# Kernel optimization log

Hardware: AMD Instinct MI355X
Metric: run time of the kernel (lower is better)

Reference implementation:

```python
import jax, jax.numpy as jnp
import numpy as np

D_MODEL = 1024
D_INNER = 2048      # expand=2 * d_model
HEADDIM = 64
NHEADS = D_INNER // HEADDIM   # 32 (ssm heads)
D_STATE = 128
D_CONV = 4
CHUNK = 256
D_IN_PROJ = 2 * D_INNER + 2 * D_STATE + NHEADS
CONV_DIM = D_INNER + 2 * D_STATE


def setup_inputs() -> dict:
    key = jax.random.key(0)
    ks = jax.random.split(key, 8)
    sc = lambda f: 1.0 / np.sqrt(f)
    dt_init = jax.random.uniform(ks[3], (NHEADS,), minval=0.001, maxval=0.1)
    return {
        "x": jax.random.normal(ks[0], (2, 4096, D_MODEL), jnp.float32),
        "W_in": jax.random.normal(ks[1], (D_MODEL, D_IN_PROJ), jnp.float32) * sc(D_MODEL),
        "conv_w": jax.random.normal(ks[2], (CONV_DIM, D_CONV), jnp.float32) * sc(D_CONV),
        "conv_b": jnp.zeros((CONV_DIM,), jnp.float32),
        "dt_bias": jnp.log(jnp.expm1(dt_init)),            # inverse softplus
        "A_log": jnp.log(jax.random.uniform(ks[4], (NHEADS,), minval=1.0, maxval=16.0)),
        "D": jnp.ones((NHEADS,), jnp.float32),
        "norm_w": jnp.ones((D_INNER,), jnp.float32),
        "W_out": jax.random.normal(ks[5], (D_INNER, D_MODEL), jnp.float32) * sc(D_INNER),
    }


def _segsum(a):
    # a: (..., T) -> (..., T, T) lower-triangular segment sums, -inf above diag
    T = a.shape[-1]
    cs = jnp.cumsum(a, axis=-1)
    diff = cs[..., :, None] - cs[..., None, :]
    mask = jnp.tril(jnp.ones((T, T), bool))
    return jnp.where(mask, diff, -jnp.inf)


def _ssd(x, A, B, C):
    # x: (b,L,h,p) already scaled by dt; A: (b,L,h) = dt*A_head; B,C: (b,L,n)
    b, L, h, p = x.shape
    nc = L // CHUNK
    xc = x.reshape(b, nc, CHUNK, h, p)
    Ac = A.reshape(b, nc, CHUNK, h).transpose(0, 3, 1, 2)      # (b,h,nc,cl)
    Bc = B.reshape(b, nc, CHUNK, -1)
    Cc = C.reshape(b, nc, CHUNK, -1)
    Acs = jnp.cumsum(Ac, axis=-1)
    # intra-chunk (diagonal) term
    Ldec = jnp.exp(_segsum(Ac))                                # (b,h,nc,cl,cl)
    Yd = jnp.einsum('bcln,bcsn,bhcls,bcshp->bclhp', Cc, Bc, Ldec, xc)
    # chunk end states
    decay_states = jnp.exp(Acs[..., -1:] - Acs)                # (b,h,nc,cl)
    states = jnp.einsum('bcln,bhcl,bclhp->bchpn', Bc, decay_states, xc)
    # inter-chunk recurrence (zero initial state)
    states = jnp.concatenate([jnp.zeros_like(states[:, :1]), states], axis=1)
    A_chunk = jnp.pad(Acs[..., -1], ((0, 0), (0, 0), (1, 0)))  # (b,h,nc+1)
    decay_chunk = jnp.exp(_segsum(A_chunk))                    # (b,h,nc+1,nc+1)
    states = jnp.einsum('bhzc,bchpn->bzhpn', decay_chunk, states)[:, :-1]
    # state -> output term
    out_decay = jnp.exp(Acs)                                   # (b,h,nc,cl)
    Yo = jnp.einsum('bcln,bchpn,bhcl->bclhp', Cc, states, out_decay)
    return (Yd + Yo).reshape(b, L, h, p)


def reference(x, W_in, conv_w, conv_b, dt_bias, A_log, D, norm_w, W_out):
    b, L, _ = x.shape
    zxbcdt = x @ W_in                                          # (b,L,4384)
    z, xBC, dt = jnp.split(zxbcdt, [D_INNER, 2 * D_INNER + 2 * D_STATE], axis=-1)
    # causal depthwise conv1d + silu
    xp = jnp.pad(xBC, ((0, 0), (D_CONV - 1, 0), (0, 0)))
    conv = sum(xp[:, k:k + L] * conv_w[:, k] for k in range(D_CONV)) + conv_b
    xBC = jax.nn.silu(conv)
    xs, B, C = jnp.split(xBC, [D_INNER, D_INNER + D_STATE], axis=-1)
    dt = jax.nn.softplus(dt + dt_bias)                         # (b,L,h)
    A = -jnp.exp(A_log)                                        # (h,)
    xh = xs.reshape(b, L, NHEADS, HEADDIM)
    y = _ssd(xh * dt[..., None], dt * A, B, C)                 # (b,L,h,p)
    y = y + xh * D[None, None, :, None]                        # D skip per head
    y = y.reshape(b, L, D_INNER)
    # gated RMSNorm
    u = y * jax.nn.silu(z)
    u = u * jax.lax.rsqrt(jnp.mean(u * u, axis=-1, keepdims=True) + 1e-5) * norm_w
    return u @ W_out
```

## Files before the change

kernel.cpp:

```cpp
#include <hip/hip_runtime.h>
#include <math.h>

#define B_ 2
#define L_ 4096
#define DM 1024
#define DI 2048
#define HD 64
#define NH 32
#define DS 128
#define CH 256
#define NC 16
#define DPROJ 4384
#define CONVD 2304
#define NGEMM 4352

typedef unsigned short u16;
typedef unsigned int u32;
typedef __attribute__((ext_vector_type(8))) short bf16x8;
typedef __attribute__((ext_vector_type(4))) float f32x4;

__device__ __forceinline__ float silu_(float x) { return x / (1.0f + __expf(-x)); }
__device__ __forceinline__ float us2f(u16 u) {
  union { u32 i; float f; } c; c.i = ((u32)u) << 16; return c.f;
}
__device__ __forceinline__ u16 f2us(float f) {
  union { float f; u32 i; } c; c.f = f;
  u32 i = c.i;
  return (u16)((i + 0x7FFFu + ((i >> 16) & 1u)) >> 16);
}
__device__ __forceinline__ void unpack8(uint4 v, float* o) {
  o[0] = us2f(v.x & 0xffffu); o[1] = us2f(v.x >> 16);
  o[2] = us2f(v.y & 0xffffu); o[3] = us2f(v.y >> 16);
  o[4] = us2f(v.z & 0xffffu); o[5] = us2f(v.z >> 16);
  o[6] = us2f(v.w & 0xffffu); o[7] = us2f(v.w >> 16);
}
__device__ __forceinline__ bf16x8 scale8(bf16x8 a, float s) {
  bf16x8 r;
#pragma unroll
  for (int j = 0; j < 8; ++j) r[j] = (short)f2us(us2f((u16)a[j]) * s);
  return r;
}
__device__ __forceinline__ void gload16(const u16* g, u16* l) {
  __builtin_amdgcn_global_load_lds(
      (const __attribute__((address_space(1))) void*)g,
      (__attribute__((address_space(3))) void*)l, 16, 0, 0);
}

__global__ __launch_bounds__(256) void cvt_t_k(const float* __restrict__ W,
                                               u16* __restrict__ Wt,
                                               int ldW, int ldT) {
  __shared__ float tile[64][65];
  const int t = threadIdx.x;
  const int n0 = blockIdx.x * 64, k0 = blockIdx.y * 64;
#pragma unroll
  for (int i = 0; i < 16; ++i) {
    int j = i * 256 + t;
    int kk = j >> 6, nn = j & 63;
    tile[kk][nn] = W[(size_t)(k0 + kk) * ldW + n0 + nn];
  }
  __syncthreads();
#pragma unroll
  for (int i = 0; i < 16; ++i) {
    int j = i * 256 + t;
    int nn = j >> 6, kk = j & 63;
    Wt[(size_t)(n0 + nn) * ldT + k0 + kk] = f2us(tile[kk][nn]);
  }
}

template <int KDIM, int NTN, int EPI>
__global__ __launch_bounds__(256) void gemm_bf16_k(const u16* __restrict__ A,
                                                   const u16* __restrict__ Bt,
                                                   u16* __restrict__ zb,
                                                   u16* __restrict__ xraw,
                                                   float* __restrict__ outf,
                                                   int nwg) {
  __shared__ u16 pool[(EPI == 1) ? 17408 : 16384];
  u16* Al = pool;
  u16* Bl = pool + 8192;
  const int t = threadIdx.x;
  const int wv = t >> 6, lane = t & 63;
  const int fr = lane & 15, oct = lane >> 4;
  const int wr = wv >> 1, wc = wv & 1;
  const int q = nwg >> 3;
  const int wg = (blockIdx.x & 7) * q + (blockIdx.x >> 3);
  const int bm = wg / NTN, bn = wg % NTN;
  const int m0 = bm * 128, n0 = bn * 128;

  const int lr = lane >> 3, ls = lane & 7;
  const int gslot = (ls ^ lr) * 8;

  f32x4 acc[4][4];
#pragma unroll
  for (int mm = 0; mm < 4; ++mm)
#pragma unroll
    for (int nn = 0; nn < 4; ++nn) acc[mm][nn] = (f32x4){0.f, 0.f, 0.f, 0.f};

  for (int k0 = 0; k0 < KDIM; k0 += 64) {
    if (k0) __syncthreads();
#pragma unroll
    for (int i = 0; i < 4; ++i) {
      const int rowA = wv * 32 + i * 8;
      gload16(&A[(size_t)(m0 + rowA + lr) * KDIM + k0 + gslot], &Al[rowA * 64]);
      gload16(&Bt[(size_t)(n0 + rowA + lr) * KDIM + k0 + gslot], &Bl[rowA * 64]);
    }
    __syncthreads();
#pragma unroll
    for (int kk = 0; kk < 2; ++kk) {
      bf16x8 af[4], bfr[4];
#pragma unroll
      for (int mm = 0; mm < 4; ++mm)
        af[mm] = *(const bf16x8*)&Al[(wr * 64 + mm * 16 + fr) * 64 +
                                     (((kk * 4 + oct) ^ (fr & 7)) * 8)];
#pragma unroll
      for (int nn = 0; nn < 4; ++nn)
        bfr[nn] = *(const bf16x8*)&Bl[(wc * 64 + nn * 16 + fr) * 64 +
                                      (((kk * 4 + oct) ^ (fr & 7)) * 8)];
#pragma unroll
      for (int mm = 0; mm < 4; ++mm)
#pragma unroll
        for (int nn = 0; nn < 4; ++nn)
          acc[mm][nn] = __builtin_amdgcn_mfma_f32_16x16x32_bf16(af[mm], bfr[nn],
                                                                acc[mm][nn], 0, 0, 0);
    }
  }

  if (EPI == 0) {
    const bool isz = (n0 < DI);
#pragma unroll
    for (int P = 0; P < 2; ++P) {
      __syncthreads();
      u16* Oh = pool;
      if (wr == P) {
#pragma unroll
        for (int mm = 0; mm < 4; ++mm)
#pragma unroll
          for (int i = 0; i < 4; ++i) {
            int rloc = mm * 16 + oct * 4 + i;
#pragma unroll
            for (int nn = 0; nn < 4; ++nn)
              Oh[rloc * 136 + wc * 64 + nn * 16 + fr] = f2us(acc[mm][nn][i]);
          }
      }
      __syncthreads();
#pragma unroll
      for (int p = 0; p < 4; ++p) {
        int e = p * 256 + t;
        int row = e >> 4, cs = (e & 15) * 8;
        uint4 v = *(const uint4*)&Oh[row * 136 + cs];
        size_t grow = m0 + P * 64 + row;
        int col = n0 + cs;
        if (isz) *(uint4*)&zb[grow * DI + col] = v;
        else     *(uint4*)&xraw[grow * CONVD + (col - DI)] = v;
      }
    }
  } else {
#pragma unroll
    for (int P = 0; P < 2; ++P) {
      __syncthreads();
      float* Of = (float*)pool;
      if (wr == P) {
#pragma unroll
        for (int mm = 0; mm < 4; ++mm)
#pragma unroll
          for (int i = 0; i < 4; ++i) {
            int rloc = mm * 16 + oct * 4 + i;
#pragma unroll
            for (int nn = 0; nn < 4; ++nn)
              Of[rloc * 132 + wc * 64 + nn * 16 + fr] = acc[mm][nn][i];
          }
      }
      __syncthreads();
#pragma unroll
      for (int p = 0; p < 8; ++p) {
        int e = p * 256 + t;
        int row = e >> 5, c4 = (e & 31) * 4;
        float4 v = *(const float4*)&Of[row * 132 + c4];
        *(float4*)&outf[(size_t)(m0 + P * 64 + row) * DM + n0 + c4] = v;
      }
    }
  }
}

__global__ __launch_bounds__(256) void dt_gemm_k(const float* __restrict__ x,
                                                 const float* __restrict__ W,
                                                 const float* __restrict__ dtb,
                                                 float* __restrict__ dtp,
                                                 u16* __restrict__ xb16) {
  __shared__ float xs[8 * 1024];
  const int t = threadIdx.x;
  const int row0 = blockIdx.x * 8;
#pragma unroll
  for (int i = 0; i < 8; ++i) {
    int j4 = i * 256 + t;
    float4 v = *(const float4*)&x[(size_t)row0 * DM + j4 * 4];
    *(float4*)&xs[j4 * 4] = v;
    u32 lo = (u32)f2us(v.x) | ((u32)f2us(v.y) << 16);
    u32 hi = (u32)f2us(v.z) | ((u32)f2us(v.w) << 16);
    *(uint2*)&xb16[(size_t)row0 * DM + j4 * 4] = make_uint2(lo, hi);
  }
  __syncthreads();
  const int r = t >> 5, h = t & 31;
  float a0 = 0.f, a1 = 0.f, a2 = 0.f, a3 = 0.f;
  const float* wcol = W + (DI + CONVD) + h;
  const float* xr = &xs[r * 1024];
  for (int k = 0; k < 1024; k += 4) {
    float4 xv = *(const float4*)&xr[k];
    a0 += xv.x * wcol[(size_t)(k + 0) * DPROJ];
    a1 += xv.y * wcol[(size_t)(k + 1) * DPROJ];
    a2 += xv.z * wcol[(size_t)(k + 2) * DPROJ];
    a3 += xv.w * wcol[(size_t)(k + 3) * DPROJ];
  }
  float v = (a0 + a1) + (a2 + a3) + dtb[h];
  dtp[(size_t)(row0 + r) * NH + h] = (v > 20.0f) ? v : log1pf(__expf(v));
}

__global__ __launch_bounds__(256) void conv_silu_k(const u16* __restrict__ xraw,
                                                   const float* __restrict__ cw,
                                                   const float* __restrict__ cb,
                                                   u16* __restrict__ xbc) {
  int idx = blockIdx.x * 256 + threadIdx.x;
  int ch8 = idx % (CONVD / 8);
  int bl = idx / (CONVD / 8);
  int l = bl & (L_ - 1);
  int ch = ch8 * 8;
  const u16* src = xraw + (size_t)bl * CONVD + ch;
  float a[8], o[8];
#pragma unroll
  for (int qq = 0; qq < 8; ++qq) a[qq] = cb[ch + qq];
  float w0[8], w1[8], w2[8], w3[8];
#pragma unroll
  for (int qq = 0; qq < 8; ++qq) {
    float4 w = *(const float4*)&cw[(ch + qq) * 4];
    w0[qq] = w.x; w1[qq] = w.y; w2[qq] = w.z; w3[qq] = w.w;
  }
  if (l >= 3) {
    uint4 v = *(const uint4*)&src[-3 * CONVD]; unpack8(v, o);
#pragma unroll
    for (int qq = 0; qq < 8; ++qq) a[qq] += o[qq] * w0[qq];
  }
  if (l >= 2) {
    uint4 v = *(const uint4*)&src[-2 * CONVD]; unpack8(v, o);
#pragma unroll
    for (int qq = 0; qq < 8; ++qq) a[qq] += o[qq] * w1[qq];
  }
  if (l >= 1) {
    uint4 v = *(const uint4*)&src[-CONVD]; unpack8(v, o);
#pragma unroll
    for (int qq = 0; qq < 8; ++qq) a[qq] += o[qq] * w2[qq];
  }
  {
    uint4 v = *(const uint4*)&src[0]; unpack8(v, o);
#pragma unroll
    for (int qq = 0; qq < 8; ++qq) a[qq] += o[qq] * w3[qq];
  }
  uint4 ov;
  ov.x = (u32)f2us(silu_(a[0])) | ((u32)f2us(silu_(a[1])) << 16);
  ov.y = (u32)f2us(silu_(a[2])) | ((u32)f2us(silu_(a[3])) << 16);
  ov.z = (u32)f2us(silu_(a[4])) | ((u32)f2us(silu_(a[5])) << 16);
  ov.w = (u32)f2us(silu_(a[6])) | ((u32)f2us(silu_(a[7])) << 16);
  *(uint4*)&xbc[(size_t)bl * CONVD + ch] = ov;
}

__global__ __launch_bounds__(256) void acs_k(const float* __restrict__ dtp,
                                             const float* __restrict__ A_log,
                                             float* __restrict__ Acs) {
  const int t = threadIdx.x;
  const int lane = t & 63, wv = t >> 6;
  const int idx = blockIdx.x * 4 + wv;
  const int h = (idx >> 4) & (NH - 1);
  const int c = idx & (NC - 1);
  const int b = idx >> 9;
  const float Ah = -__expf(A_log[h]);
  const size_t base = ((size_t)b * L_ + c * CH + lane * 4) * NH + h;
  float v0 = dtp[base] * Ah;
  float v1 = dtp[base + NH] * Ah;
  float v2 = dtp[base + 2 * NH] * Ah;
  float v3 = dtp[base + 3 * NH] * Ah;
  float c1 = v0 + v1, c2 = c1 + v2, c3 = c2 + v3;
  float tot = c3;
#pragma unroll
  for (int off = 1; off < 64; off <<= 1) {
    float p = __shfl_up(tot, off, 64);
    if (lane >= off) tot += p;
  }
  float excl = tot - c3;
  float4 ov = make_float4(excl + v0, excl + c1, excl + c2, excl + c3);
  *(float4*)&Acs[(size_t)idx * CH + lane * 4] = ov;
}

#define SLP 72
__global__ __launch_bounds__(256) void states_k(const u16* __restrict__ xbc,
                                                const float* __restrict__ dtp,
                                                const float* __restrict__ Acs,
                                                u16* __restrict__ st16) {
  __shared__ u16 BtT[128 * SLP];
  __shared__ u16 XtT[64 * SLP];
  const int t = threadIdx.x;
  const int wv = t >> 6, lane = t & 63;
  const int fr = lane & 15, oct = lane >> 4;
  const int h = blockIdx.x & 31, c = (blockIdx.x >> 5) & 15, b = blockIdx.x >> 9;
  const size_t acsb = (((size_t)b * NH + h) * NC + c) * CH;
  const float acs_last = Acs[acsb + (CH - 1)];
  const size_t rowbase = (size_t)b * L_ + c * CH;

  f32x4 acc[2][4];
#pragma unroll
  for (int mt = 0; mt < 2; ++mt)
#pragma unroll
    for (int pt = 0; pt < 4; ++pt) acc[mt][pt] = (f32x4){0.f, 0.f, 0.f, 0.f};

  for (int lt = 0; lt < 4; ++lt) {
    __syncthreads();
#pragma unroll
    for (int i = 0; i < 4; ++i) {
      int ci = i * 256 + t;
      int l = ci >> 4, nk = ci & 15;
      uint4 v = *(const uint4*)&xbc[(rowbase + lt * 64 + l) * CONVD + DI + nk * 8];
      u16 p8[8];
      p8[0] = (u16)(v.x & 0xffffu); p8[1] = (u16)(v.x >> 16);
      p8[2] = (u16)(v.y & 0xffffu); p8[3] = (u16)(v.y >> 16);
      p8[4] = (u16)(v.z & 0xffffu); p8[5] = (u16)(v.z >> 16);
      p8[6] = (u16)(v.w & 0xffffu); p8[7] = (u16)(v.w >> 16);
#pragma unroll
      for (int qq = 0; qq < 8; ++qq) {
        int r = nk * 8 + qq;
        BtT[r * SLP + ((((l >> 3) ^ (r >> 3)) & 7) << 3) + (l & 7)] = p8[qq];
      }
    }
#pragma unroll
    for (int i = 0; i < 2; ++i) {
      int ci = i * 256 + t;
      int l = ci >> 3, pk = ci & 7;
      size_t row = rowbase + lt * 64 + l;
      uint4 v = *(const uint4*)&xbc[row * CONVD + h * HD + pk * 8];
      float d = dtp[row * NH + h] * __expf(acs_last - Acs[acsb + lt * 64 + l]);
      float o[8]; unpack8(v, o);
#pragma unroll
      for (int qq = 0; qq < 8; ++qq) {
        int r = pk * 8 + qq;
        XtT[r * SLP + ((((l >> 3) ^ (r >> 3)) & 7) << 3) + (l & 7)] = f2us(o[qq] * d);
      }
    }
    __syncthreads();
    __builtin_amdgcn_s_setprio(1);
#pragma unroll
    for (int ks = 0; ks < 2; ++ks) {
      bf16x8 afr[2], bfr[4];
#pragma unroll
      for (int mt = 0; mt < 2; ++mt) {
        int r = wv * 32 + mt * 16 + fr;
        afr[mt] = *(const bf16x8*)&BtT[r * SLP + ((((ks * 4 + oct) ^ (r >> 3)) & 7) << 3)];
      }
#pragma unroll
      for (int pt = 0; pt < 4; ++pt) {
        int r = pt * 16 + fr;
        bfr[pt] = *(const bf16x8*)&XtT[r * SLP + ((((ks * 4 + oct) ^ (r >> 3)) & 7) << 3)];
      }
#pragma unroll
      for (int mt = 0; mt < 2; ++mt)
#pragma unroll
        for (int pt = 0; pt < 4; ++pt)
          acc[mt][pt] = __builtin_amdgcn_mfma_f32_16x16x32_bf16(afr[mt], bfr[pt],
                                                                acc[mt][pt], 0, 0, 0);
    }
    __builtin_amdgcn_s_setprio(0);
  }
  size_t sbase = (((size_t)b * NC + c) * NH + h) * (size_t)(HD * DS);
#pragma unroll
  for (int mt = 0; mt < 2; ++mt)
#pragma unroll
    for (int pt = 0; pt < 4; ++pt) {
      int p = pt * 16 + fr;
      int n0 = wv * 32 + mt * 16 + oct * 4;
      u32 lo = (u32)f2us(acc[mt][pt][0]) | ((u32)f2us(acc[mt][pt][1]) << 16);
      u32 hi = (u32)f2us(acc[mt][pt][2]) | ((u32)f2us(acc[mt][pt][3]) << 16);
      *(uint2*)&st16[sbase + (size_t)p * DS + n0] = make_uint2(lo, hi);
    }
}

__global__ __launch_bounds__(256) void scan_k(u16* __restrict__ st16,
                                              const float* __restrict__ Acs) {
  const int t = threadIdx.x;
  const int seg = blockIdx.x & 15;
  const int bh = blockIdx.x >> 4;
  const int h = bh & 31, b = bh >> 5;
  const int e2 = seg * 256 + t;
  const size_t acssb = ((size_t)b * NH + h) * NC * CH;
  float run0 = 0.0f, run1 = 0.0f;
#pragma unroll
  for (int c = 0; c < NC; ++c) {
    float dAl = __expf(Acs[acssb + (size_t)c * CH + (CH - 1)]);
    size_t e = (((size_t)b * NC + c) * NH + h) * (size_t)(HD * DS) + e2 * 2;
    u32 v = *(const u32*)&st16[e];
    float s0 = us2f((u16)(v & 0xffffu)), s1 = us2f((u16)(v >> 16));
    *(u32*)&st16[e] = (u32)f2us(run0) | ((u32)f2us(run1) << 16);
    run0 = fmaf(dAl, run0, s0);
    run1 = fmaf(dAl, run1, s1);
  }
}

#define SP 72
#define XOFF 8192
#define POFF 12800
__global__ __launch_bounds__(512, 4) void ssd_out_k(const u16* __restrict__ xbc,
                                                    const float* __restrict__ dtp,
                                                    const float* __restrict__ Acs,
                                                    const u16* __restrict__ st16,
                                                    const float* __restrict__ Dvec,
                                                    u16* __restrict__ y) {
  __shared__ u16 pool[31232];
  __shared__ float acs_s[256];
  const int t = threadIdx.x;
  const int w = t >> 6, lane = t & 63;
  const int fr = lane & 15, oct = lane >> 4;
  const int h = blockIdx.x & 31, c = (blockIdx.x >> 5) & 15, b = blockIdx.x >> 9;
  const size_t acsb = (((size_t)b * NH + h) * NC + c) * CH;
  const size_t rowbase = (size_t)b * L_ + c * CH;
  if (t < 256) acs_s[t] = Acs[acsb + t];
  const size_t sb = (((size_t)b * NC + c) * NH + h) * (size_t)(HD * DS);
#pragma unroll
  for (int i = 0; i < 2; ++i) {
    int ci = i * 512 + t; int p = ci >> 4, nk = ci & 15;
    uint4 v = *(const uint4*)&st16[sb + (size_t)p * DS + nk * 8];
    *(uint4*)&pool[p * 136 + nk * 8] = v;
  }
  __syncthreads();
  bf16x8 ca[2][4];
#pragma unroll
  for (int mt = 0; mt < 2; ++mt)
#pragma unroll
    for (int kk = 0; kk < 4; ++kk)
      ca[mt][kk] = *(const bf16x8*)&xbc[(rowbase + w * 32 + mt * 16 + fr) * CONVD +
                                        DI + DS + kk * 32 + oct * 8];
  f32x4 acc_y[2][4];
#pragma unroll
  for (int mt = 0; mt < 2; ++mt)
#pragma unroll
    for (int pp4 = 0; pp4 < 4; ++pp4) acc_y[mt][pp4] = (f32x4){0.f, 0.f, 0.f, 0.f};

  {
    float eL0 = __expf(acs_s[w * 32 + fr]);
    float eL1 = __expf(acs_s[w * 32 + 16 + fr]);
    __builtin_amdgcn_s_setprio(1);
#pragma unroll
    for (int kk = 0; kk < 4; ++kk) {
      bf16x8 c0 = scale8(ca[0][kk], eL0);
      bf16x8 c1 = scale8(ca[1][kk], eL1);
#pragma unroll
      for (int pp4 = 0; pp4 < 4; ++pp4) {
        bf16x8 sf = *(const bf16x8*)&pool[(pp4 * 16 + fr) * 136 + kk * 32 + oct * 8];
        acc_y[0][pp4] = __builtin_amdgcn_mfma_f32_16x16x32_bf16(c0, sf, acc_y[0][pp4], 0, 0, 0);
        acc_y[1][pp4] = __builtin_amdgcn_mfma_f32_16x16x32_bf16(c1, sf, acc_y[1][pp4], 0, 0, 0);
      }
    }
    __builtin_amdgcn_s_setprio(0);
  }

  const int stmax = w >> 1, delta = (w & 1) << 5;
  for (int st = 0; st < 4; ++st) {
    __syncthreads();
#pragma unroll
    for (int i = 0; i < 2; ++i) {
      int ci = i * 512 + t; int ll = ci >> 4, ck = ci & 15;
      uint4 v = *(const uint4*)&xbc[(rowbase + st * 64 + ll) * CONVD + DI + ck * 8];
      *(uint4*)&pool[ll * 128 + ((ck * 8) ^ ((ll & 7) << 3))] = v;
    }
    {
      int s = t >> 3, pk = t & 7;
      size_t row = rowbase + st * 64 + s;
      uint4 v = *(const uint4*)&xbc[row * CONVD + h * HD + pk * 8];
      float d = dtp[row * NH + h];
      float o[8]; unpack8(v, o);
#pragma unroll
      for (int qq = 0; qq < 8; ++qq) {
        int r = pk * 8 + qq;
        pool[XOFF + r * SP + ((((s >> 3) ^ (r >> 3)) & 7) << 3) + (s & 7)] = f2us(o[qq] * d);
      }
    }
    __syncthreads();
    if (st > stmax) continue;
    const bool diag = (st == stmax);
#pragma unroll
    for (int ss4 = 0; ss4 < 4; ++ss4) {
      bf16x8 bbf[4];
#pragma unroll
      for (int kk = 0; kk < 4; ++kk)
        bbf[kk] = *(const bf16x8*)&pool[(ss4 * 16 + fr) * 128 +
                                        ((kk * 32 + oct * 8) ^ ((fr & 7) << 3))];
      int s_in = ss4 * 16 + fr;
      float aS = acs_s[st * 64 + s_in];
#pragma unroll
      for (int mt = 0; mt < 2; ++mt) {
        f32x4 sacc = (f32x4){0.f, 0.f, 0.f, 0.f};
        __builtin_amdgcn_s_setprio(1);
#pragma unroll
        for (int kk = 0; kk < 4; ++kk)
          sacc = __builtin_amdgcn_mfma_f32_16x16x32_bf16(ca[mt][kk], bbf[kk], sacc, 0, 0, 0);
        __builtin_amdgcn_s_setprio(0);
#pragma unroll
        for (int i = 0; i < 4; ++i) {
          int r = mt * 16 + oct * 4 + i;
          float aL = acs_s[w * 32 + r];
          float wgt = (!diag || (s_in <= r + delta)) ? __expf(aL - aS) : 0.0f;
          pool[POFF + w * 2304 + r * SP + s_in] = f2us(sacc[i] * wgt);
        }
      }
    }
    bf16x8 pa[2][2];
#pragma unroll
    for (int mt = 0; mt < 2; ++mt)
#pragma unroll
      for (int k2 = 0; k2 < 2; ++k2)
        pa[mt][k2] = *(const bf16x8*)&pool[POFF + w * 2304 + (mt * 16 + fr) * SP +
                                           k2 * 32 + oct * 8];
    __builtin_amdgcn_s_setprio(1);
#pragma unroll
    for (int pp4 = 0; pp4 < 4; ++pp4) {
      int rx = pp4 * 16 + fr, xg = rx >> 3;
      bf16x8 xb0 = *(const bf16x8*)&pool[XOFF + rx * SP + (((oct) ^ xg) & 7) * 8];
      bf16x8 xb1 = *(const bf16x8*)&pool[XOFF + rx * SP + (((4 + oct) ^ xg) & 7) * 8];
#pragma unroll
      for (int mt = 0; mt < 2; ++mt) {
        acc_y[mt][pp4] = __builtin_amdgcn_mfma_f32_16x16x32_bf16(pa[mt][0], xb0, acc_y[mt][pp4], 0, 0, 0);
        acc_y[mt][pp4] = __builtin_amdgcn_mfma_f32_16x16x32_bf16(pa[mt][1], xb1, acc_y[mt][pp4], 0, 0, 0);
      }
    }
    __builtin_amdgcn_s_setprio(0);
  }

  const float Dh = Dvec[h];
#pragma unroll
  for (int mt = 0; mt < 2; ++mt)
#pragma unroll
    for (int i = 0; i < 4; ++i) {
      size_t row = rowbase + w * 32 + mt * 16 + oct * 4 + i;
#pragma unroll
      for (int pp4 = 0; pp4 < 4; ++pp4) {
        int col = h * HD + pp4 * 16 + fr;
        float xs = us2f(xbc[row * CONVD + col]);
        y[row * DI + col] = f2us(acc_y[mt][pp4][i] + Dh * xs);
      }
    }
}

__global__ __launch_bounds__(256) void gnorm_k(const u16* __restrict__ zb,
                                               const float* __restrict__ nw,
                                               u16* __restrict__ y) {
  const int row = blockIdx.x, t = threadIdx.x;
  const u16* zr = zb + (size_t)row * DI;
  u16* yr = y + (size_t)row * DI;
  uint4 zv = *(const uint4*)&zr[t * 8];
  uint4 yv = *(const uint4*)&yr[t * 8];
  float uz[8], uy[8];
  unpack8(zv, uz); unpack8(yv, uy);
  float u[8], ssum = 0.0f;
#pragma unroll
  for (int j = 0; j < 8; ++j) { u[j] = uy[j] * silu_(uz[j]); ssum += u[j] * u[j]; }
#pragma unroll
  for (int off = 32; off >= 1; off >>= 1) ssum += __shfl_xor(ssum, off, 64);
  __shared__ float red[4];
  if ((t & 63) == 0) red[t >> 6] = ssum;
  __syncthreads();
  float sc = rsqrtf((red[0] + red[1] + red[2] + red[3]) * (1.0f / DI) + 1e-5f);
  float4 w0 = *(const float4*)&nw[t * 8];
  float4 w1 = *(const float4*)&nw[t * 8 + 4];
  float o0 = u[0] * sc * w0.x, o1 = u[1] * sc * w0.y, o2 = u[2] * sc * w0.z, o3 = u[3] * sc * w0.w;
  float o4 = u[4] * sc * w1.x, o5 = u[5] * sc * w1.y, o6 = u[6] * sc * w1.z, o7 = u[7] * sc * w1.w;
  uint4 ov;
  ov.x = (u32)f2us(o0) | ((u32)f2us(o1) << 16);
  ov.y = (u32)f2us(o2) | ((u32)f2us(o3) << 16);
  ov.z = (u32)f2us(o4) | ((u32)f2us(o5) << 16);
  ov.w = (u32)f2us(o6) | ((u32)f2us(o7) << 16);
  *(uint4*)&yr[t * 8] = ov;
}

extern "C" void kernel_launch(void* const* d_in, const int* in_sizes, int n_in,
                              void* d_out, int out_size, void* d_ws, size_t ws_size,
                              hipStream_t stream) {
  const float* x      = (const float*)d_in[0];
  const float* W_in   = (const float*)d_in[1];
  const float* conv_w = (const float*)d_in[2];
  const float* conv_b = (const float*)d_in[3];
  const float* dt_b   = (const float*)d_in[4];
  const float* A_log  = (const float*)d_in[5];
  const float* Dvec   = (const float*)d_in[6];
  const float* norm_w = (const float*)d_in[7];
  const float* W_out  = (const float*)d_in[8];
  float* out = (float*)d_out;

  u16* zb       = (u16*)d_ws;
  u16* xbc      = zb + (size_t)B_ * L_ * DI;
  float* dtp    = (float*)(xbc + (size_t)B_ * L_ * CONVD);
  float* Acs    = dtp + (size_t)B_ * L_ * NH;
  u16* stregion = (u16*)(Acs + (size_t)B_ * NH * L_);
  u16* uni      = stregion + (size_t)B_ * NC * NH * HD * DS * 2;
  u16* xraw = uni;
  u16* y    = uni;

  u16* xb16     = stregion;
  u16* wint     = stregion + (size_t)B_ * L_ * DM;
  u16* states16 = stregion;
  u16* woutt    = stregion;

  const int Mrows = B_ * L_;

  dt_gemm_k<<<Mrows / 8, 256, 0, stream>>>(x, W_in, dt_b, dtp, xb16);
  cvt_t_k<<<dim3(NGEMM / 64, DM / 64), 256, 0, stream>>>(W_in, wint, DPROJ, DM);

  const int nwg_in = (Mrows / 128) * (NGEMM / 128);
  gemm_bf16_k<DM, NGEMM / 128, 0><<<nwg_in, 256, 0, stream>>>(
      xb16, wint, zb, xraw, nullptr, nwg_in);

  conv_silu_k<<<(Mrows * (CONVD / 8)) / 256, 256, 0, stream>>>(xraw, conv_w, conv_b, xbc);
  acs_k<<<(B_ * NH * NC) / 4, 256, 0, stream>>>(dtp, A_log, Acs);
  states_k<<<B_ * NC * NH, 256, 0, stream>>>(xbc, dtp, Acs, states16);
  scan_k<<<B_ * NH * 16, 256, 0, stream>>>(states16, Acs);
  ssd_out_k<<<B_ * NC * NH, 512, 0, stream>>>(xbc, dtp, Acs, states16, Dvec, y);
  gnorm_k<<<Mrows, 256, 0, stream>>>(zb, norm_w, y);

  cvt_t_k<<<dim3(DM / 64, DI / 64), 256, 0, stream>>>(W_out, woutt, DM, DI);
  const int nwg_out = (Mrows / 128) * (DM / 128);
  gemm_bf16_k<DI, DM / 128, 1><<<nwg_out, 256, 0, stream>>>(
      y, woutt, nullptr, nullptr, out, nwg_out);
}
```

Before: 348.1 us.

## Use 256x128 tiles for input GEMM and pair-row packed LDS transposes

Adds a dedicated in-projection GEMM kernel with 512-thread blocks computing 256x128 output tiles, so each B tile is reused across twice as many rows, and raises MFMA wave priority during the math. In states_k and ssd_out_k, each thread now handles two consecutive rows and writes packed 32-bit pairs into the transposed LDS tiles, halving the number of scattered 16-bit LDS stores. Both kernels also remap block indices with an XCD-style swizzle. The larger GEMM tile uses more LDS and registers per block, which may lower occupancy.

```diff
diff --git a/kernel.cpp b/kernel.cpp
--- a/kernel.cpp
+++ b/kernel.cpp
@@ -34,6 +34,12 @@
   o[4] = us2f(v.z & 0xffffu); o[5] = us2f(v.z >> 16);
   o[6] = us2f(v.w & 0xffffu); o[7] = us2f(v.w >> 16);
 }
+__device__ __forceinline__ void unpk16(uint4 v, u16* o) {
+  o[0] = (u16)(v.x & 0xffffu); o[1] = (u16)(v.x >> 16);
+  o[2] = (u16)(v.y & 0xffffu); o[3] = (u16)(v.y >> 16);
+  o[4] = (u16)(v.z & 0xffffu); o[5] = (u16)(v.z >> 16);
+  o[6] = (u16)(v.w & 0xffffu); o[7] = (u16)(v.w >> 16);
+}
 __device__ __forceinline__ bf16x8 scale8(bf16x8 a, float s) {
   bf16x8 r;
 #pragma unroll
@@ -67,14 +73,102 @@
   }
 }
 
-template <int KDIM, int NTN, int EPI>
+__global__ __launch_bounds__(512, 4) void gemm_in_k(const u16* __restrict__ A,
+                                                    const u16* __restrict__ Bt,
+                                                    u16* __restrict__ zb,
+                                                    u16* __restrict__ xraw,
+                                                    int nwg) {
+  __shared__ u16 pool[24576];
+  u16* Al = pool;
+  u16* Bl = pool + 16384;
+  const int t = threadIdx.x;
+  const int w = t >> 6, lane = t & 63;
+  const int fr = lane & 15, oct = lane >> 4;
+  const int wm = w >> 1, wn = w & 1;
+  const int q = nwg >> 3;
+  const int wg = (blockIdx.x & 7) * q + (blockIdx.x >> 3);
+  const int bm = wg / (NGEMM / 128), bn = wg % (NGEMM / 128);
+  const int m0 = bm * 256, n0 = bn * 128;
+  const int lr = lane >> 3, ls = lane & 7;
+  const int gslot = (ls ^ lr) * 8;
+
+  f32x4 acc[4][4];
+#pragma unroll
+  for (int mm = 0; mm < 4; ++mm)
+#pragma unroll
+    for (int nn = 0; nn < 4; ++nn) acc[mm][nn] = (f32x4){0.f, 0.f, 0.f, 0.f};
+
+  for (int k0 = 0; k0 < DM; k0 += 64) {
+    if (k0) __syncthreads();
+#pragma unroll
+    for (int i = 0; i < 4; ++i) {
+      const int rowA = w * 32 + i * 8;
+      gload16(&A[(size_t)(m0 + rowA + lr) * DM + k0 + gslot], &Al[rowA * 64]);
+    }
+#pragma unroll
+    for (int i = 0; i < 2; ++i) {
+      const int rowB = w * 16 + i * 8;
+      gload16(&Bt[(size_t)(n0 + rowB + lr) * DM + k0 + gslot], &Bl[rowB * 64]);
+    }
+    __syncthreads();
+#pragma unroll
+    for (int kk = 0; kk < 2; ++kk) {
+      bf16x8 af[4], bfr[4];
+#pragma unroll
+      for (int mm = 0; mm < 4; ++mm)
+        af[mm] = *(const bf16x8*)&Al[(wm * 64 + mm * 16 + fr) * 64 +
+                                     (((kk * 4 + oct) ^ (fr & 7)) * 8)];
+#pragma unroll
+      for (int nn = 0; nn < 4; ++nn)
+        bfr[nn] = *(const bf16x8*)&Bl[(wn * 64 + nn * 16 + fr) * 64 +
+                                      (((kk * 4 + oct) ^ (fr & 7)) * 8)];
+      __builtin_amdgcn_s_setprio(1);
+#pragma unroll
+      for (int mm = 0; mm < 4; ++mm)
+#pragma unroll
+        for (int nn = 0; nn < 4; ++nn)
+          acc[mm][nn] = __builtin_amdgcn_mfma_f32_16x16x32_bf16(af[mm], bfr[nn],
+                                                                acc[mm][nn], 0, 0, 0);
+      __builtin_amdgcn_s_setprio(0);
+    }
+  }
+
+  const bool isz = (n0 < DI);
+  u16* Oh = pool;
+#pragma unroll
+  for (int P = 0; P < 4; ++P) {
+    __syncthreads();
+    if (wm == P) {
+#pragma unroll
+      for (int mm = 0; mm < 4; ++mm)
+#pragma unroll
+        for (int i = 0; i < 4; ++i) {
+          int rloc = mm * 16 + oct * 4 + i;
+#pragma unroll
+          for (int nn = 0; nn < 4; ++nn)
+            Oh[rloc * 136 + wn * 64 + nn * 16 + fr] = f2us(acc[mm][nn][i]);
+        }
+    }
+    __syncthreads();
+#pragma unroll
+    for (int p = 0; p < 2; ++p) {
+      int e = p * 512 + t;
+      int row = e >> 4, cs = (e & 15) * 8;
+      uint4 v = *(const uint4*)&Oh[row * 136 + cs];
+      size_t grow = m0 + P * 64 + row;
+      int col = n0 + cs;
+      if (isz) *(uint4*)&zb[grow * DI + col] = v;
+      else     *(uint4*)&xraw[grow * CONVD + (col - DI)] = v;
+    }
+  }
+}
+
+template <int KDIM, int NTN>
 __global__ __launch_bounds__(256) void gemm_bf16_k(const u16* __restrict__ A,
                                                    const u16* __restrict__ Bt,
-                                                   u16* __restrict__ zb,
-                                                   u16* __restrict__ xraw,
                                                    float* __restrict__ outf,
                                                    int nwg) {
-  __shared__ u16 pool[(EPI == 1) ? 17408 : 16384];
+  __shared__ u16 pool[17408];
   u16* Al = pool;
   u16* Bl = pool + 8192;
   const int t = threadIdx.x;
@@ -124,59 +218,28 @@
     }
   }
 
-  if (EPI == 0) {
-    const bool isz = (n0 < DI);
-#pragma unroll
-    for (int P = 0; P < 2; ++P) {
-      __syncthreads();
-      u16* Oh = pool;
-      if (wr == P) {
-#pragma unroll
-        for (int mm = 0; mm < 4; ++mm)
-#pragma unroll
-          for (int i = 0; i < 4; ++i) {
-            int rloc = mm * 16 + oct * 4 + i;
-#pragma unroll
-            for (int nn = 0; nn < 4; ++nn)
-              Oh[rloc * 136 + wc * 64 + nn * 16 + fr] = f2us(acc[mm][nn][i]);
-          }
-      }
-      __syncthreads();
-#pragma unroll
-      for (int p = 0; p < 4; ++p) {
-        int e = p * 256 + t;
-        int row = e >> 4, cs = (e & 15) * 8;
-        uint4 v = *(const uint4*)&Oh[row * 136 + cs];
-        size_t grow = m0 + P * 64 + row;
-        int col = n0 + cs;
-        if (isz) *(uint4*)&zb[grow * DI + col] = v;
-        else     *(uint4*)&xraw[grow * CONVD + (col - DI)] = v;
-      }
-    }
-  } else {
-#pragma unroll
-    for (int P = 0; P < 2; ++P) {
-      __syncthreads();
-      float* Of = (float*)pool;
-      if (wr == P) {
-#pragma unroll
-        for (int mm = 0; mm < 4; ++mm)
-#pragma unroll
-          for (int i = 0; i < 4; ++i) {
-            int rloc = mm * 16 + oct * 4 + i;
-#pragma unroll
-            for (int nn = 0; nn < 4; ++nn)
-              Of[rloc * 132 + wc * 64 + nn * 16 + fr] = acc[mm][nn][i];
-          }
-      }
-      __syncthreads();
-#pragma unroll
-      for (int p = 0; p < 8; ++p) {
-        int e = p * 256 + t;
-        int row = e >> 5, c4 = (e & 31) * 4;
-        float4 v = *(const float4*)&Of[row * 132 + c4];
-        *(float4*)&outf[(size_t)(m0 + P * 64 + row) * DM + n0 + c4] = v;
-      }
+#pragma unroll
+  for (int P = 0; P < 2; ++P) {
+    __syncthreads();
+    float* Of = (float*)pool;
+    if (wr == P) {
+#pragma unroll
+      for (int mm = 0; mm < 4; ++mm)
+#pragma unroll
+        for (int i = 0; i < 4; ++i) {
+          int rloc = mm * 16 + oct * 4 + i;
+#pragma unroll
+          for (int nn = 0; nn < 4; ++nn)
+            Of[rloc * 132 + wc * 64 + nn * 16 + fr] = acc[mm][nn][i];
+        }
+    }
+    __syncthreads();
+#pragma unroll
+    for (int p = 0; p < 8; ++p) {
+      int e = p * 256 + t;
+      int row = e >> 5, c4 = (e & 31) * 4;
+      float4 v = *(const float4*)&Of[row * 132 + c4];
+      *(float4*)&outf[(size_t)(m0 + P * 64 + row) * DM + n0 + c4] = v;
     }
   }
 }
@@ -298,7 +361,8 @@
   const int t = threadIdx.x;
   const int wv = t >> 6, lane = t & 63;
   const int fr = lane & 15, oct = lane >> 4;
-  const int h = blockIdx.x & 31, c = (blockIdx.x >> 5) & 15, b = blockIdx.x >> 9;
+  const int sw = (blockIdx.x & 7) * 128 + (blockIdx.x >> 3);
+  const int h = sw & 31, c = (sw >> 5) & 15, b = sw >> 9;
   const size_t acsb = (((size_t)b * NH + h) * NC + c) * CH;
   const float acs_last = Acs[acsb + (CH - 1)];
   const size_t rowbase = (size_t)b * L_ + c * CH;
@@ -312,33 +376,37 @@
   for (int lt = 0; lt < 4; ++lt) {
     __syncthreads();
 #pragma unroll
-    for (int i = 0; i < 4; ++i) {
+    for (int i = 0; i < 2; ++i) {
       int ci = i * 256 + t;
-      int l = ci >> 4, nk = ci & 15;
-      uint4 v = *(const uint4*)&xbc[(rowbase + lt * 64 + l) * CONVD + DI + nk * 8];
-      u16 p8[8];
-      p8[0] = (u16)(v.x & 0xffffu); p8[1] = (u16)(v.x >> 16);
-      p8[2] = (u16)(v.y & 0xffffu); p8[3] = (u16)(v.y >> 16);
-      p8[4] = (u16)(v.z & 0xffffu); p8[5] = (u16)(v.z >> 16);
-      p8[6] = (u16)(v.w & 0xffffu); p8[7] = (u16)(v.w >> 16);
+      int lp = ci >> 4, nk = ci & 15;
+      int l0 = lp * 2;
+      const u16* srcp = &xbc[(rowbase + lt * 64 + l0) * CONVD + DI + nk * 8];
+      uint4 v0 = *(const uint4*)srcp;
+      uint4 v1 = *(const uint4*)(srcp + CONVD);
+      u16 a0[8], a1[8];
+      unpk16(v0, a0); unpk16(v1, a1);
 #pragma unroll
       for (int qq = 0; qq < 8; ++qq) {
         int r = nk * 8 + qq;
-        BtT[r * SLP + ((((l >> 3) ^ (r >> 3)) & 7) << 3) + (l & 7)] = p8[qq];
-      }
-    }
-#pragma unroll
-    for (int i = 0; i < 2; ++i) {
-      int ci = i * 256 + t;
-      int l = ci >> 3, pk = ci & 7;
-      size_t row = rowbase + lt * 64 + l;
-      uint4 v = *(const uint4*)&xbc[row * CONVD + h * HD + pk * 8];
-      float d = dtp[row * NH + h] * __expf(acs_last - Acs[acsb + lt * 64 + l]);
-      float o[8]; unpack8(v, o);
+        u32 val = (u32)a0[qq] | ((u32)a1[qq] << 16);
+        *(u32*)&BtT[r * SLP + ((((l0 >> 3) ^ (r >> 3)) & 7) << 3) + (l0 & 7)] = val;
+      }
+    }
+    {
+      int lp = t >> 3, pk = t & 7;
+      int l0 = lp * 2;
+      size_t row0 = rowbase + lt * 64 + l0;
+      uint4 v0 = *(const uint4*)&xbc[row0 * CONVD + h * HD + pk * 8];
+      uint4 v1 = *(const uint4*)&xbc[(row0 + 1) * CONVD + h * HD + pk * 8];
+      float d0 = dtp[row0 * NH + h] * __expf(acs_last - Acs[acsb + lt * 64 + l0]);
+      float d1 = dtp[(row0 + 1) * NH + h] * __expf(acs_last - Acs[acsb + lt * 64 + l0 + 1]);
+      float o0[8], o1[8];
+      unpack8(v0, o0); unpack8(v1, o1);
 #pragma unroll
       for (int qq = 0; qq < 8; ++qq) {
         int r = pk * 8 + qq;
-        XtT[r * SLP + ((((l >> 3) ^ (r >> 3)) & 7) << 3) + (l & 7)] = f2us(o[qq] * d);
+        u32 val = (u32)f2us(o0[qq] * d0) | ((u32)f2us(o1[qq] * d1) << 16);
+        *(u32*)&XtT[r * SLP + ((((l0 >> 3) ^ (r >> 3)) & 7) << 3) + (l0 & 7)] = val;
       }
     }
     __syncthreads();
@@ -413,7 +481,8 @@
   const int t = threadIdx.x;
   const int w = t >> 6, lane = t & 63;
   const int fr = lane & 15, oct = lane >> 4;
-  const int h = blockIdx.x & 31, c = (blockIdx.x >> 5) & 15, b = blockIdx.x >> 9;
+  const int sw = (blockIdx.x & 7) * 128 + (blockIdx.x >> 3);
+  const int h = sw & 31, c = (sw >> 5) & 15, b = sw >> 9;
   const size_t acsb = (((size_t)b * NH + h) * NC + c) * CH;
   const size_t rowbase = (size_t)b * L_ + c * CH;
   if (t < 256) acs_s[t] = Acs[acsb + t];
@@ -465,16 +534,21 @@
       uint4 v = *(const uint4*)&xbc[(rowbase + st * 64 + ll) * CONVD + DI + ck * 8];
       *(uint4*)&pool[ll * 128 + ((ck * 8) ^ ((ll & 7) << 3))] = v;
     }
-    {
-      int s = t >> 3, pk = t & 7;
-      size_t row = rowbase + st * 64 + s;
-      uint4 v = *(const uint4*)&xbc[row * CONVD + h * HD + pk * 8];
-      float d = dtp[row * NH + h];
-      float o[8]; unpack8(v, o);
+    if (t < 256) {
+      int lp = t >> 3, pk = t & 7;
+      int s0 = lp * 2;
+      size_t row0 = rowbase + st * 64 + s0;
+      uint4 v0 = *(const uint4*)&xbc[row0 * CONVD + h * HD + pk * 8];
+      uint4 v1 = *(const uint4*)&xbc[(row0 + 1) * CONVD + h * HD + pk * 8];
+      float d0 = dtp[row0 * NH + h];
+      float d1 = dtp[(row0 + 1) * NH + h];
+      float o0[8], o1[8];
+      unpack8(v0, o0); unpack8(v1, o1);
 #pragma unroll
       for (int qq = 0; qq < 8; ++qq) {
         int r = pk * 8 + qq;
-        pool[XOFF + r * SP + ((((s >> 3) ^ (r >> 3)) & 7) << 3) + (s & 7)] = f2us(o[qq] * d);
+        u32 val = (u32)f2us(o0[qq] * d0) | ((u32)f2us(o1[qq] * d1) << 16);
+        *(u32*)&pool[XOFF + r * SP + ((((s0 >> 3) ^ (r >> 3)) & 7) << 3) + (s0 & 7)] = val;
       }
     }
     __syncthreads();
@@ -607,9 +681,8 @@
   dt_gemm_k<<<Mrows / 8, 256, 0, stream>>>(x, W_in, dt_b, dtp, xb16);
   cvt_t_k<<<dim3(NGEMM / 64, DM / 64), 256, 0, stream>>>(W_in, wint, DPROJ, DM);
 
-  const int nwg_in = (Mrows / 128) * (NGEMM / 128);
-  gemm_bf16_k<DM, NGEMM / 128, 0><<<nwg_in, 256, 0, stream>>>(
-      xb16, wint, zb, xraw, nullptr, nwg_in);
+  const int nwg_in = (Mrows / 256) * (NGEMM / 128);
+  gemm_in_k<<<nwg_in, 512, 0, stream>>>(xb16, wint, zb, xraw, nwg_in);
 
   conv_silu_k<<<(Mrows * (CONVD / 8)) / 256, 256, 0, stream>>>(xraw, conv_w, conv_b, xbc);
   acs_k<<<(B_ * NH * NC) / 4, 256, 0, stream>>>(dtp, A_log, Acs);
@@ -620,6 +693,5 @@
 
   cvt_t_k<<<dim3(DM / 64, DI / 64), 256, 0, stream>>>(W_out, woutt, DM, DI);
   const int nwg_out = (Mrows / 128) * (DM / 128);
-  gemm_bf16_k<DI, DM / 128, 1><<<nwg_out, 256, 0, stream>>>(
-      y, woutt, nullptr, nullptr, out, nwg_out);
-}
+  gemm_bf16_k<DI, DM / 128><<<nwg_out, 256, 0, stream>>>(y, woutt, out, nwg_out);
+}
```

Result: no change. 345.9 us (-0.6%).
